# Performance work log

Measured on AMD Instinct MI355X. Metric: run time of the kernel, lower is better.

Reference implementation:

```python
import jax, jax.numpy as jnp
import numpy as np


def _gla_forward(hidden_state, Wq, bq, Wk, bk, Wv, bv, Wg, bg, Wo, bo):
    # hidden_state: (B, T, H)
    q = hidden_state @ Wq + bq                       # (B, T, K)
    k = jax.nn.sigmoid(hidden_state @ Wk + bk)       # (B, T, K)
    g = jax.nn.sigmoid(hidden_state @ Wg + bg)       # (B, T, K)
    v = hidden_state @ Wv + bv                       # (B, T, V)

    B = hidden_state.shape[0]
    K = Wq.shape[1]
    V = Wv.shape[1]
    state0 = jnp.zeros((B, K, V), dtype=hidden_state.dtype)

    def step(state, inp):
        q_t, k_t, g_t, v_t = inp                     # (B,K),(B,K),(B,K),(B,V)
        # state = state * gate[..., None] + k outer v
        state = state * g_t[:, :, None] + k_t[:, :, None] * v_t[:, None, :]
        out_t = jnp.einsum('bkv,bk->bv', state, q_t)  # (B, V)
        return state, out_t

    # scan over time: move T to leading axis
    xs = (jnp.swapaxes(q, 0, 1), jnp.swapaxes(k, 0, 1),
          jnp.swapaxes(g, 0, 1), jnp.swapaxes(v, 0, 1))
    final_state, outs = jax.lax.scan(step, state0, xs)  # outs: (T, B, V)
    out = jnp.swapaxes(outs, 0, 1)                      # (B, T, V)
    out = out @ Wo + bo                                 # (B, T, O)
    return out, final_state


def setup_inputs() -> dict:
    key = jax.random.key(0)
    ks = jax.random.split(key, 12)
    B, T, H, K, V, O = 8, 2048, 1024, 256, 256, 1024
    s = 0.02
    return {
        'hidden_state': jax.random.normal(ks[0], (B, T, H), dtype=jnp.float32),
        'Wq': jax.random.normal(ks[1], (H, K), dtype=jnp.float32) * s,
        'bq': jax.random.normal(ks[2], (K,), dtype=jnp.float32) * s,
        'Wk': jax.random.normal(ks[3], (H, K), dtype=jnp.float32) * s,
        'bk': jax.random.normal(ks[4], (K,), dtype=jnp.float32) * s,
        'Wv': jax.random.normal(ks[5], (H, V), dtype=jnp.float32) * s,
        'bv': jax.random.normal(ks[6], (V,), dtype=jnp.float32) * s,
        'Wg': jax.random.normal(ks[7], (H, K), dtype=jnp.float32) * s,
        'bg': jax.random.normal(ks[8], (K,), dtype=jnp.float32) * s,
        'Wo': jax.random.normal(ks[9], (V, O), dtype=jnp.float32) * s,
        'bo': jax.random.normal(ks[10], (O,), dtype=jnp.float32) * s,
    }


def reference(hidden_state, Wq, bq, Wk, bk, Wv, bv, Wg, bg, Wo, bo):
    return _gla_forward(hidden_state, Wq, bq, Wk, bk, Wv, bv, Wg, bg, Wo, bo)
```

## Files before the change

kernel.cpp:

```cpp
#include <hip/hip_runtime.h>

#define Bb 8
#define Tt 2048
#define Hh 1024
#define Kk 256
#define Vv 256
#define Oo 1024
#define CC 64
#define NC 32

typedef __attribute__((ext_vector_type(8))) __bf16 bf16x8;
typedef __attribute__((ext_vector_type(4))) float f32x4;

__device__ __forceinline__ unsigned short f2b(float f) {
  unsigned u = __float_as_uint(f);
  u = (u + 0x7FFFu + ((u >> 16) & 1u)) >> 16;
  return (unsigned short)u;
}
__device__ __forceinline__ float b2f(unsigned short u) {
  return __uint_as_float(((unsigned)u) << 16);
}
__device__ __forceinline__ void gload_lds16(const unsigned short* g, unsigned short* l) {
  __builtin_amdgcn_global_load_lds(
      (const __attribute__((address_space(1))) void*)g,
      (__attribute__((address_space(3))) void*)l, 16, 0, 0);
}

__global__ __launch_bounds__(256) void cast_bf16_kernel(const float* __restrict__ in,
                                                        unsigned short* __restrict__ out,
                                                        int n4) {
  int i = blockIdx.x * 256 + threadIdx.x;
  if (i >= n4) return;
  float4 v = ((const float4*)in)[i];
  ushort4 o;
  o.x = f2b(v.x); o.y = f2b(v.y); o.z = f2b(v.z); o.w = f2b(v.w);
  ((ushort4*)out)[i] = o;
}

__global__ __launch_bounds__(256) void transpose_cast_kernel(const float* __restrict__ W,
                                                             unsigned short* __restrict__ WT,
                                                             int H, int N) {
  __shared__ float tile[32][33];
  int h0 = blockIdx.x * 32, n0 = blockIdx.y * 32;
  int tx = threadIdx.x & 31, ty = threadIdx.x >> 5;
  for (int r = ty; r < 32; r += 8)
    tile[r][tx] = W[(size_t)(h0 + r) * N + n0 + tx];
  __syncthreads();
  for (int r = ty; r < 32; r += 8)
    WT[(size_t)(n0 + r) * H + h0 + tx] = f2b(tile[tx][r]);
}

#define BM 128
#define BN 128
#define BK 64

template <int MODE>
__global__ __launch_bounds__(256, 4) void gemm_mf_kernel(
    const unsigned short* __restrict__ A, const unsigned short* __restrict__ Bt,
    const float* __restrict__ b0p, const float* __restrict__ b1p,
    const float* __restrict__ b2p, const float* __restrict__ b3p,
    float* __restrict__ Cf,
    unsigned short* __restrict__ O0, unsigned short* __restrict__ O1,
    unsigned short* __restrict__ O2, unsigned short* __restrict__ O3,
    int M, int N, int K) {
  __shared__ __align__(16) unsigned short shbuf[16384];
  unsigned short* As = shbuf;
  unsigned short* Bs = shbuf + 8192;
  const int tid = threadIdx.x;
  const int lane = tid & 63, wid = tid >> 6;
  const int wm = wid >> 1, wn = wid & 1;
  const int lin = blockIdx.x + blockIdx.y * gridDim.x;
  const int xcd = lin & 7;
  const int jj = lin >> 3;
  const int mpg = gridDim.y >> 3;
  const int m0 = (xcd * mpg + jj / gridDim.x) * BM;
  const int n0 = (jj % gridDim.x) * BN;
  const int fr = lane & 15, fq = lane >> 4;
  const int srl = lane >> 3;
  const int scs = ((lane & 7) ^ srl) * 8;
  const unsigned short* gaBase = A + (size_t)(m0 + srl) * K + scs;
  const unsigned short* gbBase = Bt + (size_t)(n0 + srl) * K + scs;

  f32x4 acc[4][4] = {};
  const int nt = K / BK;
  for (int t = 0; t < nt; ++t) {
    const int k0 = t * BK;
    __syncthreads();
#pragma unroll
    for (int inst = 0; inst < 4; ++inst) {
      const int rb = wid * 32 + inst * 8;
      gload_lds16(gaBase + (size_t)rb * K + k0, &As[rb * BK]);
      gload_lds16(gbBase + (size_t)rb * K + k0, &Bs[rb * BK]);
    }
    __syncthreads();
#pragma unroll
    for (int ks = 0; ks < 2; ++ks) {
      bf16x8 af[4], bfv[4];
#pragma unroll
      for (int j = 0; j < 4; ++j) {
        const int R = wn * 64 + j * 16 + fr;
        const int ch = ((ks << 2) | fq) ^ (fr & 7);
        bfv[j] = *(const bf16x8*)&Bs[R * BK + ch * 8];
      }
#pragma unroll
      for (int i = 0; i < 4; ++i) {
        const int R = wm * 64 + i * 16 + fr;
        const int ch = ((ks << 2) | fq) ^ (fr & 7);
        af[i] = *(const bf16x8*)&As[R * BK + ch * 8];
      }
#pragma unroll
      for (int i = 0; i < 4; ++i)
#pragma unroll
        for (int j = 0; j < 4; ++j)
          acc[i][j] = __builtin_amdgcn_mfma_f32_16x16x32_bf16(af[i], bfv[j], acc[i][j], 0, 0, 0);
    }
  }
  if (MODE == 1) {
#pragma unroll
    for (int j = 0; j < 4; ++j) {
      const int n = n0 + wn * 64 + j * 16 + fr;
      const float bv = b0p[n];
#pragma unroll
      for (int i = 0; i < 4; ++i) {
        const int mb = m0 + wm * 64 + i * 16 + fq * 4;
#pragma unroll
        for (int r = 0; r < 4; ++r)
          Cf[(size_t)(mb + r) * N + n] = acc[i][j][r] + bv;
      }
    }
  } else {
    __syncthreads();
    const int sel = n0 >> 8;
    const float* bp = sel == 0 ? b0p : sel == 1 ? b1p : sel == 2 ? b2p : b3p;
#pragma unroll
    for (int j = 0; j < 4; ++j) {
      const int ncol = wn * 64 + j * 16 + fr;
      const int nloc = (n0 & 255) + ncol;
      const float bv = bp[nloc];
#pragma unroll
      for (int i = 0; i < 4; ++i) {
#pragma unroll
        for (int r = 0; r < 4; ++r) {
          const int ml = wm * 64 + i * 16 + fq * 4 + r;
          const float x = acc[i][j][r] + bv;
          unsigned short us;
          if (sel == 0) {
            us = f2b(x);
          } else if (sel == 1) {
            us = f2b(1.f / (1.f + expf(-x)));
          } else if (sel == 2) {
            float e = exp2f(-x * 1.44269504f);
            float lg = -log2f(1.f + e);
            _Float16 hv = (_Float16)lg;
            __builtin_memcpy(&us, &hv, 2);
          } else {
            us = f2b(x);
          }
          if (sel == 3) {
            const int cm = (ml >> 3) ^ (ncol & 15);
            shbuf[ncol * 128 + cm * 8 + (ml & 7)] = us;
          } else {
            const int cn = (ncol >> 3) ^ (ml & 15);
            shbuf[ml * 128 + cn * 8 + (ncol & 7)] = us;
          }
        }
      }
    }
    __syncthreads();
    const int row = tid >> 1;
    const int half = tid & 1;
    if (sel == 3) {
      unsigned short* dst = O3 + ((size_t)(m0 >> 11) * Vv + (n0 & 255) + row) * Tt +
                            (m0 & 2047) + half * 64;
#pragma unroll
      for (int ic = 0; ic < 8; ++ic) {
        const int chunk = half * 8 + ic;
        const int sc = chunk ^ (row & 15);
        *(uint4*)(dst + ic * 8) = *(const uint4*)&shbuf[row * 128 + sc * 8];
      }
    } else {
      unsigned short* Op = sel == 0 ? O0 : sel == 1 ? O1 : O2;
      unsigned short* dst = Op + (size_t)(m0 + row) * 256 + (n0 & 255) + half * 64;
#pragma unroll
      for (int ic = 0; ic < 8; ++ic) {
        const int chunk = half * 8 + ic;
        const int sc = chunk ^ (row & 15);
        *(uint4*)(dst + ic * 8) = *(const uint4*)&shbuf[row * 128 + sc * 8];
      }
    }
  }
}

__global__ __launch_bounds__(256) void prep_sgemm_kernel(
    const unsigned short* __restrict__ qb, const unsigned short* __restrict__ kb,
    const unsigned short* __restrict__ lgb, const unsigned short* __restrict__ vTb,
    unsigned short* __restrict__ q2b, unsigned short* __restrict__ qab,
    unsigned short* __restrict__ kab,
    float* __restrict__ LBb, float* __restrict__ Dendb,
    unsigned short* __restrict__ Sb) {
  __shared__ __align__(16) unsigned short khs[256][72];
  const int c = blockIdx.x, b = blockIdx.y;
  const int k = threadIdx.x;
  const int task = b * NC + c;
  const size_t rowbase = ((size_t)b * Tt + (size_t)c * CC) * Kk + k;
  float Ls = 0.f;
  float LBr[4];
#pragma unroll
  for (int gq = 0; gq < 4; ++gq) {
    LBr[gq] = Ls;
#pragma unroll
    for (int tt = 0; tt < 16; ++tt) {
      int t = gq * 16 + tt;
      _Float16 hv;
      __builtin_memcpy(&hv, &lgb[rowbase + (size_t)t * Kk], 2);
      Ls += (float)hv;
    }
  }
  const float Lend = Ls;
#pragma unroll
  for (int gq = 0; gq < 4; ++gq) LBb[(size_t)task * 1024 + gq * 256 + k] = LBr[gq];
  Dendb[task * 256 + k] = exp2f(Lend);
  float L = 0.f;
#pragma unroll
  for (int gq = 0; gq < 4; ++gq) {
    const float LBc = LBr[gq];
    unsigned kw[8];
#pragma unroll
    for (int tt = 0; tt < 16; ++tt) {
      int t = gq * 16 + tt;
      size_t off = rowbase + (size_t)t * Kk;
      _Float16 hv;
      __builtin_memcpy(&hv, &lgb[off], 2);
      L += (float)hv;
      float qv = b2f(qb[off]);
      float kv = b2f(kb[off]);
      q2b[off] = f2b(qv * exp2f(L));
      qab[off] = f2b(qv * exp2f(L - LBc));
      kab[off] = f2b(kv * exp2f(LBc - L));
      unsigned short kh = f2b(kv * exp2f(Lend - L));
      if (tt & 1) kw[tt >> 1] |= ((unsigned)kh) << 16;
      else        kw[tt >> 1] = kh;
    }
    uint4 u0; u0.x = kw[0]; u0.y = kw[1]; u0.z = kw[2]; u0.w = kw[3];
    uint4 u1; u1.x = kw[4]; u1.y = kw[5]; u1.z = kw[6]; u1.w = kw[7];
    *(uint4*)&khs[k][gq * 16] = u0;
    *(uint4*)&khs[k][gq * 16 + 8] = u1;
  }
  __syncthreads();
  const int tid = threadIdx.x, lane = tid & 63, w = tid >> 6;
  const int fr = lane & 15, fq = lane >> 4, fk = fq * 8;
  const unsigned short* vt = vTb + (size_t)b * (Vv * Tt) + (size_t)c * CC;
  for (int vb4 = 0; vb4 < 4; ++vb4) {
    f32x4 acc[4][4] = {};
#pragma unroll
    for (int ks = 0; ks < 2; ++ks) {
      bf16x8 af[4], bf[4];
#pragma unroll
      for (int i = 0; i < 4; ++i)
        af[i] = *(const bf16x8*)&khs[w * 64 + i * 16 + fr][ks * 32 + fk];
#pragma unroll
      for (int j = 0; j < 4; ++j)
        bf[j] = *(const bf16x8*)(vt + (size_t)(vb4 * 64 + j * 16 + fr) * Tt + ks * 32 + fk);
#pragma unroll
      for (int i = 0; i < 4; ++i)
#pragma unroll
        for (int j = 0; j < 4; ++j)
          acc[i][j] = __builtin_amdgcn_mfma_f32_16x16x32_bf16(af[i], bf[j], acc[i][j], 0, 0, 0);
    }
#pragma unroll
    for (int i = 0; i < 4; ++i)
#pragma unroll
      for (int j = 0; j < 4; ++j)
#pragma unroll
        for (int r = 0; r < 4; ++r)
          Sb[(size_t)task * (Kk * Vv) + (size_t)(w * 64 + i * 16 + fq * 4 + r) * Vv +
             vb4 * 64 + j * 16 + fr] = f2b(acc[i][j][r]);
  }
}

__global__ __launch_bounds__(256) void passR_kernel(
    const unsigned short* __restrict__ Sb, const float* __restrict__ Dendb,
    unsigned short* __restrict__ S0Tb, float* __restrict__ state_out) {
  const int vt = blockIdx.x, kt = blockIdx.y, b = blockIdx.z;
  const int tid = threadIdx.x;
  const int kq = tid >> 2;
  const int vq = tid & 3;
  const int vr = tid >> 3;
  const int kqq = tid & 7;
  __shared__ __align__(16) unsigned short Ts[32][72];
  float st[8];
#pragma unroll
  for (int j = 0; j < 8; ++j) st[j] = 0.f;
  for (int c = 0; c < NC; ++c) {
    const int task = b * NC + c;
#pragma unroll
    for (int j = 0; j < 8; ++j) Ts[vq * 8 + j][kq] = f2b(st[j]);
    __syncthreads();
    {
      unsigned short* dst = S0Tb + (size_t)task * (Kk * Vv) +
                            (size_t)(vt * 32 + vr) * Kk + kt * 64 + kqq * 8;
      *(uint4*)dst = *(const uint4*)&Ts[vr][kqq * 8];
    }
    __syncthreads();
    const float d = Dendb[task * 256 + kt * 64 + kq];
    const unsigned short* sp = Sb + (size_t)task * (Kk * Vv) +
                               (size_t)(kt * 64 + kq) * Vv + vt * 32 + vq * 8;
    uint4 raw = *(const uint4*)sp;
    unsigned ws_[4] = {raw.x, raw.y, raw.z, raw.w};
#pragma unroll
    for (int e = 0; e < 4; ++e) {
      float lo = __uint_as_float(ws_[e] << 16);
      float hi = __uint_as_float(ws_[e] & 0xFFFF0000u);
      st[e * 2]     = d * st[e * 2] + lo;
      st[e * 2 + 1] = d * st[e * 2 + 1] + hi;
    }
  }
  float* so = state_out + (size_t)(b * Kk + kt * 64 + kq) * Vv + vt * 32 + vq * 8;
#pragma unroll
  for (int j = 0; j < 8; ++j) so[j] = st[j];
}

__global__ __launch_bounds__(256) void passO_kernel(
    const unsigned short* __restrict__ qab, const unsigned short* __restrict__ kab,
    const unsigned short* __restrict__ q2b, const float* __restrict__ LBb,
    const unsigned short* __restrict__ S0Tb, const unsigned short* __restrict__ vTb,
    unsigned short* __restrict__ attb) {
  const int c = blockIdx.x, b = blockIdx.y;
  const int task = b * NC + c;
  const int tid = threadIdx.x, lane = tid & 63, w = tid >> 6;
  const int fr = lane & 15, fq = lane >> 4, fk = fq * 8;
  __shared__ float LB_s[4][256];
  __shared__ float D_s[6][256];
  __shared__ __align__(16) unsigned short A_s[64][72];
  const size_t tbase = (size_t)task * (CC * Kk);
  for (int idx = tid; idx < 1024; idx += 256) LB_s[idx >> 8][idx & 255] = LBb[(size_t)task * 1024 + idx];
  for (int idx = tid; idx < 64 * 72 / 2; idx += 256) ((unsigned*)A_s)[idx] = 0;
  __syncthreads();
  {
    const int kk = tid;
#pragma unroll
    for (int pi = 0; pi < 6; ++pi) {
      const int I = (pi >= 3) ? 3 : (pi >= 1) ? 2 : 1;
      const int J = pi - (I * (I - 1)) / 2;
      D_s[pi][kk] = exp2f(LB_s[I][kk] - LB_s[J][kk]);
    }
  }
  __syncthreads();
  for (int p = w; p < 10; p += 4) {
    const int I = (p >= 6) ? 3 : (p >= 3) ? 2 : (p >= 1) ? 1 : 0;
    const int J = p - (I * (I + 1)) / 2;
    const int pidx = (I * (I - 1)) / 2 + J;
    f32x4 acc = {0.f, 0.f, 0.f, 0.f};
#pragma unroll
    for (int ks = 0; ks < 8; ++ks) {
      const int k0 = ks * 32 + fk;
      bf16x8 af = *(const bf16x8*)(qab + tbase + (size_t)(I * 16 + fr) * Kk + k0);
      if (I != J) {
#pragma unroll
        for (int e = 0; e < 8; ++e)
          af[e] = (__bf16)((float)af[e] * D_s[pidx][k0 + e]);
      }
      bf16x8 bf = *(const bf16x8*)(kab + tbase + (size_t)(J * 16 + fr) * Kk + k0);
      acc = __builtin_amdgcn_mfma_f32_16x16x32_bf16(af, bf, acc, 0, 0, 0);
    }
#pragma unroll
    for (int r = 0; r < 4; ++r) {
      const int ml = fq * 4 + r, nl = fr;
      bool keep = (I != J) || (nl <= ml);
      A_s[I * 16 + ml][J * 16 + nl] = keep ? f2b(acc[r]) : (unsigned short)0;
    }
  }
  __syncthreads();
  f32x4 acc2[4][4] = {};
  const unsigned short* q2t = q2b + tbase;
  const unsigned short* s0t = S0Tb + (size_t)task * (Kk * Vv);
  const unsigned short* vtp = vTb + (size_t)b * (Vv * Tt) + (size_t)c * CC;
  const int vbase = w * 64;
#pragma unroll
  for (int ks = 0; ks < 8; ++ks) {
    const int k0 = ks * 32 + fk;
    bf16x8 af[4], bf[4];
#pragma unroll
    for (int i = 0; i < 4; ++i) af[i] = *(const bf16x8*)(q2t + (size_t)(i * 16 + fr) * Kk + k0);
#pragma unroll
    for (int j = 0; j < 4; ++j) bf[j] = *(const bf16x8*)(s0t + (size_t)(vbase + j * 16 + fr) * Kk + k0);
#pragma unroll
    for (int i = 0; i < 4; ++i)
#pragma unroll
      for (int j = 0; j < 4; ++j)
        acc2[i][j] = __builtin_amdgcn_mfma_f32_16x16x32_bf16(af[i], bf[j], acc2[i][j], 0, 0, 0);
  }
#pragma unroll
  for (int ks = 0; ks < 2; ++ks) {
    const int s0 = ks * 32 + fk;
    bf16x8 af[4], bf[4];
#pragma unroll
    for (int i = 0; i < 4; ++i) af[i] = *(const bf16x8*)&A_s[i * 16 + fr][s0];
#pragma unroll
    for (int j = 0; j < 4; ++j) bf[j] = *(const bf16x8*)(vtp + (size_t)(vbase + j * 16 + fr) * Tt + s0);
#pragma unroll
    for (int i = 0; i < 4; ++i)
#pragma unroll
      for (int j = 0; j < 4; ++j)
        acc2[i][j] = __builtin_amdgcn_mfma_f32_16x16x32_bf16(af[i], bf[j], acc2[i][j], 0, 0, 0);
  }
#pragma unroll
  for (int i = 0; i < 4; ++i)
#pragma unroll
    for (int j = 0; j < 4; ++j)
#pragma unroll
      for (int r = 0; r < 4; ++r)
        attb[((size_t)b * Tt + c * CC + i * 16 + fq * 4 + r) * Vv + vbase + j * 16 + fr]
            = f2b(acc2[i][j][r]);
}

extern "C" void kernel_launch(void* const* d_in, const int* in_sizes, int n_in,
                              void* d_out, int out_size, void* d_ws, size_t ws_size,
                              hipStream_t stream) {
  const float* hs = (const float*)d_in[0];
  const float* Wq = (const float*)d_in[1];
  const float* bq = (const float*)d_in[2];
  const float* Wk = (const float*)d_in[3];
  const float* bk = (const float*)d_in[4];
  const float* Wv = (const float*)d_in[5];
  const float* bv = (const float*)d_in[6];
  const float* Wg = (const float*)d_in[7];
  const float* bg = (const float*)d_in[8];
  const float* Wo = (const float*)d_in[9];
  const float* bo = (const float*)d_in[10];

  float* out = (float*)d_out;
  float* state_out = out + (size_t)Bb * Tt * Oo;

  char* p = (char*)d_ws;
  auto alloc = [&](size_t bytes) {
    char* r = p;
    p += (bytes + 255) & ~(size_t)255;
    return r;
  };
  unsigned short* hsb   = (unsigned short*)alloc((size_t)Bb * Tt * Hh * 2);
  unsigned short* WallT = (unsigned short*)alloc((size_t)1024 * Hh * 2);
  unsigned short* WoT   = (unsigned short*)alloc((size_t)Oo * Vv * 2);
  unsigned short* qb    = (unsigned short*)alloc((size_t)Bb * Tt * Kk * 2);
  unsigned short* kb    = (unsigned short*)alloc((size_t)Bb * Tt * Kk * 2);
  unsigned short* lgb   = (unsigned short*)alloc((size_t)Bb * Tt * Kk * 2);
  unsigned short* vTb   = (unsigned short*)alloc((size_t)Bb * Vv * Tt * 2);
  unsigned short* attb  = (unsigned short*)alloc((size_t)Bb * Tt * Vv * 2);
  unsigned short* q2b   = (unsigned short*)alloc((size_t)Bb * Tt * Kk * 2);
  unsigned short* qab   = (unsigned short*)alloc((size_t)Bb * Tt * Kk * 2);
  unsigned short* kab   = (unsigned short*)alloc((size_t)Bb * Tt * Kk * 2);
  float*          LBb   = (float*)alloc((size_t)Bb * NC * 4 * Kk * 4);
  float*          Dendb = (float*)alloc((size_t)Bb * NC * Kk * 4);
  unsigned short* Sb    = (unsigned short*)alloc((size_t)Bb * NC * Kk * Vv * 2);
  unsigned short* S0Tb  = (unsigned short*)alloc((size_t)Bb * NC * Kk * Vv * 2);

  int n4 = Bb * Tt * Hh / 4;
  cast_bf16_kernel<<<(n4 + 255) / 256, 256, 0, stream>>>(hs, hsb, n4);
  transpose_cast_kernel<<<dim3(Hh / 32, Kk / 32), 256, 0, stream>>>(Wq, WallT + 0 * Kk * Hh, Hh, Kk);
  transpose_cast_kernel<<<dim3(Hh / 32, Kk / 32), 256, 0, stream>>>(Wk, WallT + 1 * Kk * Hh, Hh, Kk);
  transpose_cast_kernel<<<dim3(Hh / 32, Kk / 32), 256, 0, stream>>>(Wg, WallT + 2 * Kk * Hh, Hh, Kk);
  transpose_cast_kernel<<<dim3(Hh / 32, Kk / 32), 256, 0, stream>>>(Wv, WallT + 3 * Kk * Hh, Hh, Kk);
  transpose_cast_kernel<<<dim3(Vv / 32, Oo / 32), 256, 0, stream>>>(Wo, WoT, Vv, Oo);

  gemm_mf_kernel<0><<<dim3(1024 / BN, (Bb * Tt) / BM), 256, 0, stream>>>(
      hsb, WallT, bq, bk, bg, bv, nullptr, qb, kb, lgb, vTb, Bb * Tt, 1024, Hh);

  prep_sgemm_kernel<<<dim3(NC, Bb), 256, 0, stream>>>(qb, kb, lgb, vTb, q2b, qab, kab,
                                                      LBb, Dendb, Sb);

  passR_kernel<<<dim3(Vv / 32, Kk / 64, Bb), 256, 0, stream>>>(Sb, Dendb, S0Tb, state_out);

  passO_kernel<<<dim3(NC, Bb), 256, 0, stream>>>(qab, kab, q2b, LBb, S0Tb, vTb, attb);

  gemm_mf_kernel<1><<<dim3(Oo / BN, (Bb * Tt) / BM), 256, 0, stream>>>(
      attb, WoT, bo, nullptr, nullptr, nullptr, out, nullptr, nullptr, nullptr, nullptr,
      Bb * Tt, Oo, Vv);
}
```

Baseline: 218.5 us.

## Rewrite projection GEMM as 8-wave 256x128 tile with triple-buffered async loads

The bf16 MFMA GEMM now uses 512-thread blocks computing 256x128 tiles. Global-to-LDS loads go into a three-slot ring buffer prefetched two K-steps ahead, split into two halves interleaved with MFMA phases. Explicit vmcnt waits, barriers and setprio raise MFMA issue priority. The aim is to hide load latency and raise data reuse per block, at the cost of 144KB LDS per block, lower occupancy, and halved grid size for these GEMMs.

Result: slower. 265.9 us (+21.7%).

```diff
diff --git a/kernel.cpp b/kernel.cpp
--- a/kernel.cpp
+++ b/kernel.cpp
@@ -50,12 +50,12 @@
     WT[(size_t)(n0 + r) * H + h0 + tx] = f2b(tile[tx][r]);
 }
 
-#define BM 128
+#define BM 256
 #define BN 128
 #define BK 64
 
 template <int MODE>
-__global__ __launch_bounds__(256, 4) void gemm_mf_kernel(
+__global__ __launch_bounds__(512, 2) void gemm8_kernel(
     const unsigned short* __restrict__ A, const unsigned short* __restrict__ Bt,
     const float* __restrict__ b0p, const float* __restrict__ b1p,
     const float* __restrict__ b2p, const float* __restrict__ b3p,
@@ -63,9 +63,9 @@
     unsigned short* __restrict__ O0, unsigned short* __restrict__ O1,
     unsigned short* __restrict__ O2, unsigned short* __restrict__ O3,
     int M, int N, int K) {
-  __shared__ __align__(16) unsigned short shbuf[16384];
-  unsigned short* As = shbuf;
-  unsigned short* Bs = shbuf + 8192;
+  __shared__ __align__(16) unsigned short shbuf[73728];
+  unsigned short* shA = shbuf;
+  unsigned short* shB = shbuf + 49152;
   const int tid = threadIdx.x;
   const int lane = tid & 63, wid = tid >> 6;
   const int wm = wid >> 1, wn = wid & 1;
@@ -80,41 +80,81 @@
   const int scs = ((lane & 7) ^ srl) * 8;
   const unsigned short* gaBase = A + (size_t)(m0 + srl) * K + scs;
   const unsigned short* gbBase = Bt + (size_t)(n0 + srl) * K + scs;
+  const int nt = K / BK;
+
+#define SA(q, tt, slot)                                                       \
+  gload_lds16(gaBase + (size_t)((q) * 64 + wid * 8) * K + (size_t)(tt) * BK,  \
+              shA + (slot) * 16384 + ((q) * 64 + wid * 8) * 64)
+#define SB(h, tt, slot)                                                       \
+  gload_lds16(gbBase + (size_t)((h) * 64 + wid * 8) * K + (size_t)(tt) * BK,  \
+              shB + (slot) * 8192 + ((h) * 64 + wid * 8) * 64)
+
+  SA(0, 0, 0); SA(1, 0, 0); SA(2, 0, 0); SA(3, 0, 0); SB(0, 0, 0); SB(1, 0, 0);
+  SA(0, 1, 1); SA(1, 1, 1); SA(2, 1, 1); SA(3, 1, 1); SB(0, 1, 1); SB(1, 1, 1);
+  asm volatile("s_waitcnt vmcnt(6)\n\ts_barrier" ::: "memory");
 
   f32x4 acc[4][4] = {};
-  const int nt = K / BK;
   for (int t = 0; t < nt; ++t) {
-    const int k0 = t * BK;
-    __syncthreads();
-#pragma unroll
-    for (int inst = 0; inst < 4; ++inst) {
-      const int rb = wid * 32 + inst * 8;
-      gload_lds16(gaBase + (size_t)rb * K + k0, &As[rb * BK]);
-      gload_lds16(gbBase + (size_t)rb * K + k0, &Bs[rb * BK]);
-    }
-    __syncthreads();
-#pragma unroll
-    for (int ks = 0; ks < 2; ++ks) {
-      bf16x8 af[4], bfv[4];
-#pragma unroll
-      for (int j = 0; j < 4; ++j) {
-        const int R = wn * 64 + j * 16 + fr;
-        const int ch = ((ks << 2) | fq) ^ (fr & 7);
-        bfv[j] = *(const bf16x8*)&Bs[R * BK + ch * 8];
-      }
-#pragma unroll
-      for (int i = 0; i < 4; ++i) {
-        const int R = wm * 64 + i * 16 + fr;
-        const int ch = ((ks << 2) | fq) ^ (fr & 7);
-        af[i] = *(const bf16x8*)&As[R * BK + ch * 8];
-      }
-#pragma unroll
-      for (int i = 0; i < 4; ++i)
-#pragma unroll
-        for (int j = 0; j < 4; ++j)
-          acc[i][j] = __builtin_amdgcn_mfma_f32_16x16x32_bf16(af[i], bfv[j], acc[i][j], 0, 0, 0);
-    }
-  }
+    const int scur = t % 3;
+    const int spre = (t + 2) % 3;
+    const bool dstage = (t + 2) < nt;
+    const unsigned short* As = shA + scur * 16384;
+    const unsigned short* Bsl = shB + scur * 8192;
+    bf16x8 af[4][2], bfv[2][2];
+    if (dstage) { SA(0, t + 2, spre); SA(1, t + 2, spre); SB(0, t + 2, spre); }
+#pragma unroll
+    for (int i = 0; i < 4; ++i) {
+      const int r = wm * 64 + i * 16 + fr;
+#pragma unroll
+      for (int ks = 0; ks < 2; ++ks)
+        af[i][ks] = *(const bf16x8*)&As[r * 64 + (((ks << 2) | fq) ^ (r & 7)) * 8];
+    }
+#pragma unroll
+    for (int jx = 0; jx < 2; ++jx) {
+      const int cc = wn * 64 + jx * 16 + fr;
+#pragma unroll
+      for (int ks = 0; ks < 2; ++ks)
+        bfv[jx][ks] = *(const bf16x8*)&Bsl[cc * 64 + (((ks << 2) | fq) ^ (cc & 7)) * 8];
+    }
+    asm volatile("s_waitcnt lgkmcnt(0)" ::: "memory");
+    __builtin_amdgcn_sched_barrier(0);
+    __builtin_amdgcn_s_setprio(1);
+#pragma unroll
+    for (int i = 0; i < 4; ++i)
+#pragma unroll
+      for (int jx = 0; jx < 2; ++jx)
+#pragma unroll
+        for (int ks = 0; ks < 2; ++ks)
+          acc[i][jx] = __builtin_amdgcn_mfma_f32_16x16x32_bf16(af[i][ks], bfv[jx][ks],
+                                                               acc[i][jx], 0, 0, 0);
+    __builtin_amdgcn_s_setprio(0);
+    asm volatile("s_barrier" ::: "memory");
+    if (dstage) { SA(2, t + 2, spre); SA(3, t + 2, spre); SB(1, t + 2, spre); }
+#pragma unroll
+    for (int jx = 0; jx < 2; ++jx) {
+      const int cc = wn * 64 + (2 + jx) * 16 + fr;
+#pragma unroll
+      for (int ks = 0; ks < 2; ++ks)
+        bfv[jx][ks] = *(const bf16x8*)&Bsl[cc * 64 + (((ks << 2) | fq) ^ (cc & 7)) * 8];
+    }
+    asm volatile("s_waitcnt lgkmcnt(0)" ::: "memory");
+    __builtin_amdgcn_sched_barrier(0);
+    __builtin_amdgcn_s_setprio(1);
+#pragma unroll
+    for (int i = 0; i < 4; ++i)
+#pragma unroll
+      for (int jx = 0; jx < 2; ++jx)
+#pragma unroll
+        for (int ks = 0; ks < 2; ++ks)
+          acc[i][2 + jx] = __builtin_amdgcn_mfma_f32_16x16x32_bf16(af[i][ks], bfv[jx][ks],
+                                                                   acc[i][2 + jx], 0, 0, 0);
+    __builtin_amdgcn_s_setprio(0);
+    if (dstage) asm volatile("s_waitcnt vmcnt(6)\n\ts_barrier" ::: "memory");
+    else        asm volatile("s_waitcnt vmcnt(0)\n\ts_barrier" ::: "memory");
+  }
+#undef SA
+#undef SB
+
   if (MODE == 1) {
 #pragma unroll
     for (int j = 0; j < 4; ++j) {
@@ -129,14 +169,12 @@
       }
     }
   } else {
-    __syncthreads();
     const int sel = n0 >> 8;
     const float* bp = sel == 0 ? b0p : sel == 1 ? b1p : sel == 2 ? b2p : b3p;
 #pragma unroll
     for (int j = 0; j < 4; ++j) {
       const int ncol = wn * 64 + j * 16 + fr;
-      const int nloc = (n0 & 255) + ncol;
-      const float bv = bp[nloc];
+      const float bv = bp[(n0 & 255) + ncol];
 #pragma unroll
       for (int i = 0; i < 4; ++i) {
 #pragma unroll
@@ -157,8 +195,8 @@
             us = f2b(x);
           }
           if (sel == 3) {
-            const int cm = (ml >> 3) ^ (ncol & 15);
-            shbuf[ncol * 128 + cm * 8 + (ml & 7)] = us;
+            const int cm = (ml >> 3) ^ (ncol & 31);
+            shbuf[ncol * 256 + cm * 8 + (ml & 7)] = us;
           } else {
             const int cn = (ncol >> 3) ^ (ml & 15);
             shbuf[ml * 128 + cn * 8 + (ncol & 7)] = us;
@@ -167,19 +205,21 @@
       }
     }
     __syncthreads();
-    const int row = tid >> 1;
-    const int half = tid & 1;
     if (sel == 3) {
+      const int row = tid >> 2;
+      const int q4 = tid & 3;
       unsigned short* dst = O3 + ((size_t)(m0 >> 11) * Vv + (n0 & 255) + row) * Tt +
-                            (m0 & 2047) + half * 64;
+                            (m0 & 2047) + q4 * 64;
 #pragma unroll
       for (int ic = 0; ic < 8; ++ic) {
-        const int chunk = half * 8 + ic;
-        const int sc = chunk ^ (row & 15);
-        *(uint4*)(dst + ic * 8) = *(const uint4*)&shbuf[row * 128 + sc * 8];
+        const int chunk = q4 * 8 + ic;
+        const int sc = chunk ^ (row & 31);
+        *(uint4*)(dst + ic * 8) = *(const uint4*)&shbuf[row * 256 + sc * 8];
       }
     } else {
       unsigned short* Op = sel == 0 ? O0 : sel == 1 ? O1 : O2;
+      const int row = tid >> 1;
+      const int half = tid & 1;
       unsigned short* dst = Op + (size_t)(m0 + row) * 256 + (n0 & 255) + half * 64;
 #pragma unroll
       for (int ic = 0; ic < 8; ++ic) {
@@ -462,7 +502,7 @@
   transpose_cast_kernel<<<dim3(Hh / 32, Kk / 32), 256, 0, stream>>>(Wv, WallT + 3 * Kk * Hh, Hh, Kk);
   transpose_cast_kernel<<<dim3(Vv / 32, Oo / 32), 256, 0, stream>>>(Wo, WoT, Vv, Oo);
 
-  gemm_mf_kernel<0><<<dim3(1024 / BN, (Bb * Tt) / BM), 256, 0, stream>>>(
+  gemm8_kernel<0><<<dim3(1024 / BN, (Bb * Tt) / BM), 512, 0, stream>>>(
       hsb, WallT, bq, bk, bg, bv, nullptr, qb, kb, lgb, vTb, Bb * Tt, 1024, Hh);
 
   prep_sgemm_kernel<<<dim3(NC, Bb), 256, 0, stream>>>(qb, kb, lgb, vTb, q2b, qab, kab,
@@ -472,7 +512,7 @@
 
   passO_kernel<<<dim3(NC, Bb), 256, 0, stream>>>(qab, kab, q2b, LBb, S0Tb, vTb, attb);
 
-  gemm_mf_kernel<1><<<dim3(Oo / BN, (Bb * Tt) / BM), 256, 0, stream>>>(
+  gemm8_kernel<1><<<dim3(Oo / BN, (Bb * Tt) / BM), 512, 0, stream>>>(
       attb, WoT, bo, nullptr, nullptr, nullptr, out, nullptr, nullptr, nullptr, nullptr,
       Bb * Tt, Oo, Vv);
 }
```

## Split GEMM into persistent two-tile projection kernel and LDS-staged output epilogue

Applied to the files above, without the earlier changes.

The projection GEMM now launches 512 blocks, each computing two M-tiles in sequence with a fixed XCD-aware mapping, instead of one tile per block over a 1024-block grid. The output GEMM gets its own kernel that stages the fp32 result through shared memory in two halves and writes rows with coalesced float4 stores, replacing scattered scalar stores. The aim is better L2 locality and less launch or tail cost for the projection, and wider store transactions for the output. The cost is more LDS use and extra barriers in the epilogue, plus less parallelism per launch for the projection.

After: 293.4 us. +34.3%, slower.

```diff
diff --git a/kernel.cpp b/kernel.cpp
--- a/kernel.cpp
+++ b/kernel.cpp
@@ -54,89 +54,73 @@
 #define BN 128
 #define BK 64
 
-template <int MODE>
-__global__ __launch_bounds__(256, 4) void gemm_mf_kernel(
+__global__ __launch_bounds__(256, 4) void gemm_proj_kernel(
     const unsigned short* __restrict__ A, const unsigned short* __restrict__ Bt,
     const float* __restrict__ b0p, const float* __restrict__ b1p,
     const float* __restrict__ b2p, const float* __restrict__ b3p,
-    float* __restrict__ Cf,
     unsigned short* __restrict__ O0, unsigned short* __restrict__ O1,
     unsigned short* __restrict__ O2, unsigned short* __restrict__ O3,
-    int M, int N, int K) {
+    int K) {
   __shared__ __align__(16) unsigned short shbuf[16384];
   unsigned short* As = shbuf;
   unsigned short* Bs = shbuf + 8192;
   const int tid = threadIdx.x;
   const int lane = tid & 63, wid = tid >> 6;
   const int wm = wid >> 1, wn = wid & 1;
-  const int lin = blockIdx.x + blockIdx.y * gridDim.x;
+  const int lin = blockIdx.x;
   const int xcd = lin & 7;
-  const int jj = lin >> 3;
-  const int mpg = gridDim.y >> 3;
-  const int m0 = (xcd * mpg + jj / gridDim.x) * BM;
-  const int n0 = (jj % gridDim.x) * BN;
+  const int rem = lin >> 3;
+  const int jm = rem & 7, jn = rem >> 3;
+  const int n0 = jn * 128;
+  const int sel = n0 >> 8;
+  const float* bp = sel == 0 ? b0p : sel == 1 ? b1p : sel == 2 ? b2p : b3p;
   const int fr = lane & 15, fq = lane >> 4;
   const int srl = lane >> 3;
   const int scs = ((lane & 7) ^ srl) * 8;
-  const unsigned short* gaBase = A + (size_t)(m0 + srl) * K + scs;
-  const unsigned short* gbBase = Bt + (size_t)(n0 + srl) * K + scs;
-
-  f32x4 acc[4][4] = {};
   const int nt = K / BK;
-  for (int t = 0; t < nt; ++t) {
-    const int k0 = t * BK;
-    __syncthreads();
-#pragma unroll
-    for (int inst = 0; inst < 4; ++inst) {
-      const int rb = wid * 32 + inst * 8;
-      gload_lds16(gaBase + (size_t)rb * K + k0, &As[rb * BK]);
-      gload_lds16(gbBase + (size_t)rb * K + k0, &Bs[rb * BK]);
-    }
-    __syncthreads();
-#pragma unroll
-    for (int ks = 0; ks < 2; ++ks) {
-      bf16x8 af[4], bfv[4];
-#pragma unroll
-      for (int j = 0; j < 4; ++j) {
-        const int R = wn * 64 + j * 16 + fr;
-        const int ch = ((ks << 2) | fq) ^ (fr & 7);
-        bfv[j] = *(const bf16x8*)&Bs[R * BK + ch * 8];
-      }
-#pragma unroll
-      for (int i = 0; i < 4; ++i) {
-        const int R = wm * 64 + i * 16 + fr;
-        const int ch = ((ks << 2) | fq) ^ (fr & 7);
-        af[i] = *(const bf16x8*)&As[R * BK + ch * 8];
-      }
-#pragma unroll
-      for (int i = 0; i < 4; ++i)
-#pragma unroll
-        for (int j = 0; j < 4; ++j)
-          acc[i][j] = __builtin_amdgcn_mfma_f32_16x16x32_bf16(af[i], bfv[j], acc[i][j], 0, 0, 0);
-    }
-  }
-  if (MODE == 1) {
-#pragma unroll
-    for (int j = 0; j < 4; ++j) {
-      const int n = n0 + wn * 64 + j * 16 + fr;
-      const float bv = b0p[n];
-#pragma unroll
-      for (int i = 0; i < 4; ++i) {
-        const int mb = m0 + wm * 64 + i * 16 + fq * 4;
-#pragma unroll
-        for (int r = 0; r < 4; ++r)
-          Cf[(size_t)(mb + r) * N + n] = acc[i][j][r] + bv;
-      }
-    }
-  } else {
-    __syncthreads();
-    const int sel = n0 >> 8;
-    const float* bp = sel == 0 ? b0p : sel == 1 ? b1p : sel == 2 ? b2p : b3p;
+
+  for (int h = 0; h < 2; ++h) {
+    const int m0 = (xcd * 16 + h * 8 + jm) * BM;
+    const unsigned short* gaBase = A + (size_t)(m0 + srl) * K + scs;
+    const unsigned short* gbBase = Bt + (size_t)(n0 + srl) * K + scs;
+    f32x4 acc[4][4] = {};
+    for (int t = 0; t < nt; ++t) {
+      const int k0 = t * BK;
+      __syncthreads();
+#pragma unroll
+      for (int inst = 0; inst < 4; ++inst) {
+        const int rb = wid * 32 + inst * 8;
+        gload_lds16(gaBase + (size_t)rb * K + k0, &As[rb * BK]);
+        gload_lds16(gbBase + (size_t)rb * K + k0, &Bs[rb * BK]);
+      }
+      __syncthreads();
+#pragma unroll
+      for (int ks = 0; ks < 2; ++ks) {
+        bf16x8 af[4], bfv[4];
+#pragma unroll
+        for (int j = 0; j < 4; ++j) {
+          const int R = wn * 64 + j * 16 + fr;
+          const int ch = ((ks << 2) | fq) ^ (fr & 7);
+          bfv[j] = *(const bf16x8*)&Bs[R * BK + ch * 8];
+        }
+#pragma unroll
+        for (int i = 0; i < 4; ++i) {
+          const int R = wm * 64 + i * 16 + fr;
+          const int ch = ((ks << 2) | fq) ^ (fr & 7);
+          af[i] = *(const bf16x8*)&As[R * BK + ch * 8];
+        }
+#pragma unroll
+        for (int i = 0; i < 4; ++i)
+#pragma unroll
+          for (int j = 0; j < 4; ++j)
+            acc[i][j] = __builtin_amdgcn_mfma_f32_16x16x32_bf16(af[i], bfv[j], acc[i][j], 0, 0, 0);
+      }
+    }
+    __syncthreads();
 #pragma unroll
     for (int j = 0; j < 4; ++j) {
       const int ncol = wn * 64 + j * 16 + fr;
-      const int nloc = (n0 & 255) + ncol;
-      const float bv = bp[nloc];
+      const float bv = bp[(n0 & 255) + ncol];
 #pragma unroll
       for (int i = 0; i < 4; ++i) {
 #pragma unroll
@@ -191,6 +175,86 @@
   }
 }
 
+__global__ __launch_bounds__(256, 4) void gemm_out_kernel(
+    const unsigned short* __restrict__ A, const unsigned short* __restrict__ Bt,
+    const float* __restrict__ bias, float* __restrict__ Cf,
+    int M, int N, int K) {
+  __shared__ __align__(16) float fstage[8448];
+  unsigned short* As = (unsigned short*)fstage;
+  unsigned short* Bs = As + 8192;
+  const int tid = threadIdx.x;
+  const int lane = tid & 63, wid = tid >> 6;
+  const int wm = wid >> 1, wn = wid & 1;
+  const int lin = blockIdx.x + blockIdx.y * gridDim.x;
+  const int xcd = lin & 7;
+  const int jj = lin >> 3;
+  const int mpg = gridDim.y >> 3;
+  const int m0 = (xcd * mpg + jj / gridDim.x) * BM;
+  const int n0 = (jj % gridDim.x) * BN;
+  const int fr = lane & 15, fq = lane >> 4;
+  const int srl = lane >> 3;
+  const int scs = ((lane & 7) ^ srl) * 8;
+  const unsigned short* gaBase = A + (size_t)(m0 + srl) * K + scs;
+  const unsigned short* gbBase = Bt + (size_t)(n0 + srl) * K + scs;
+
+  f32x4 acc[4][4] = {};
+  const int nt = K / BK;
+  for (int t = 0; t < nt; ++t) {
+    const int k0 = t * BK;
+    __syncthreads();
+#pragma unroll
+    for (int inst = 0; inst < 4; ++inst) {
+      const int rb = wid * 32 + inst * 8;
+      gload_lds16(gaBase + (size_t)rb * K + k0, &As[rb * BK]);
+      gload_lds16(gbBase + (size_t)rb * K + k0, &Bs[rb * BK]);
+    }
+    __syncthreads();
+#pragma unroll
+    for (int ks = 0; ks < 2; ++ks) {
+      bf16x8 af[4], bfv[4];
+#pragma unroll
+      for (int j = 0; j < 4; ++j) {
+        const int R = wn * 64 + j * 16 + fr;
+        const int ch = ((ks << 2) | fq) ^ (fr & 7);
+        bfv[j] = *(const bf16x8*)&Bs[R * BK + ch * 8];
+      }
+#pragma unroll
+      for (int i = 0; i < 4; ++i) {
+        const int R = wm * 64 + i * 16 + fr;
+        const int ch = ((ks << 2) | fq) ^ (fr & 7);
+        af[i] = *(const bf16x8*)&As[R * BK + ch * 8];
+      }
+#pragma unroll
+      for (int i = 0; i < 4; ++i)
+#pragma unroll
+        for (int j = 0; j < 4; ++j)
+          acc[i][j] = __builtin_amdgcn_mfma_f32_16x16x32_bf16(af[i], bfv[j], acc[i][j], 0, 0, 0);
+    }
+  }
+  for (int ch = 0; ch < 2; ++ch) {
+    __syncthreads();
+    if (wm == ch) {
+#pragma unroll
+      for (int j = 0; j < 4; ++j) {
+        const int col = wn * 64 + j * 16 + fr;
+        const float bv = bias[n0 + col];
+#pragma unroll
+        for (int i = 0; i < 4; ++i)
+#pragma unroll
+          for (int r = 0; r < 4; ++r)
+            fstage[(i * 16 + fq * 4 + r) * 132 + col] = acc[i][j][r] + bv;
+      }
+    }
+    __syncthreads();
+    const int rl = tid >> 2, qc = tid & 3;
+    float* dst = Cf + (size_t)(m0 + ch * 64 + rl) * N + n0 + qc * 32;
+    const float* src = fstage + rl * 132 + qc * 32;
+#pragma unroll
+    for (int e = 0; e < 8; ++e)
+      *(float4*)(dst + e * 4) = *(const float4*)(src + e * 4);
+  }
+}
+
 __global__ __launch_bounds__(256) void prep_sgemm_kernel(
     const unsigned short* __restrict__ qb, const unsigned short* __restrict__ kb,
     const unsigned short* __restrict__ lgb, const unsigned short* __restrict__ vTb,
@@ -462,8 +526,8 @@
   transpose_cast_kernel<<<dim3(Hh / 32, Kk / 32), 256, 0, stream>>>(Wv, WallT + 3 * Kk * Hh, Hh, Kk);
   transpose_cast_kernel<<<dim3(Vv / 32, Oo / 32), 256, 0, stream>>>(Wo, WoT, Vv, Oo);
 
-  gemm_mf_kernel<0><<<dim3(1024 / BN, (Bb * Tt) / BM), 256, 0, stream>>>(
-      hsb, WallT, bq, bk, bg, bv, nullptr, qb, kb, lgb, vTb, Bb * Tt, 1024, Hh);
+  gemm_proj_kernel<<<512, 256, 0, stream>>>(
+      hsb, WallT, bq, bk, bg, bv, qb, kb, lgb, vTb, Hh);
 
   prep_sgemm_kernel<<<dim3(NC, Bb), 256, 0, stream>>>(qb, kb, lgb, vTb, q2b, qab, kab,
                                                       LBb, Dendb, Sb);
@@ -472,7 +536,6 @@
 
   passO_kernel<<<dim3(NC, Bb), 256, 0, stream>>>(qab, kab, q2b, LBb, S0Tb, vTb, attb);
 
-  gemm_mf_kernel<1><<<dim3(Oo / BN, (Bb * Tt) / BM), 256, 0, stream>>>(
-      attb, WoT, bo, nullptr, nullptr, nullptr, out, nullptr, nullptr, nullptr, nullptr,
-      Bb * Tt, Oo, Vv);
-}
+  gemm_out_kernel<<<dim3(Oo / BN, (Bb * Tt) / BM), 256, 0, stream>>>(
+      attb, WoT, bo, out, Bb * Tt, Oo, Vv);
+}
```

## Double-buffer GEMM LDS tiles with BK=32 to overlap global loads with MFMA

Applied to the files above, without the earlier changes.

The bf16 MFMA GEMM now uses a K-tile of 32 and two LDS buffers in the same shared allocation. The next tile is prefetched with global_load_lds while the current one is consumed, using vmcnt waits and raw s_barrier instead of two __syncthreads per step. The swizzle is reworked for the narrower tile. The aim is to hide global-to-LDS latency, at the cost of twice as many loop iterations and tighter reliance on hand-written waitcnt ordering.

Result: slower. 223.5 us (+2.3%).

```diff
diff --git a/kernel.cpp b/kernel.cpp
--- a/kernel.cpp
+++ b/kernel.cpp
@@ -52,7 +52,7 @@
 
 #define BM 128
 #define BN 128
-#define BK 64
+#define BK 32
 
 template <int MODE>
 __global__ __launch_bounds__(256, 4) void gemm_mf_kernel(
@@ -76,37 +76,46 @@
   const int m0 = (xcd * mpg + jj / gridDim.x) * BM;
   const int n0 = (jj % gridDim.x) * BN;
   const int fr = lane & 15, fq = lane >> 4;
-  const int srl = lane >> 3;
-  const int scs = ((lane & 7) ^ srl) * 8;
+  const int srl = lane >> 2;
+  const int scs = ((lane & 3) ^ (srl & 3)) * 8;
   const unsigned short* gaBase = A + (size_t)(m0 + srl) * K + scs;
   const unsigned short* gbBase = Bt + (size_t)(n0 + srl) * K + scs;
+  const int nt = K / BK;
+
+#define STAGE(buf, tt)                                                         \
+  {                                                                            \
+    _Pragma("unroll") for (int inst = 0; inst < 2; ++inst) {                   \
+      const int rb = wid * 32 + inst * 16;                                     \
+      gload_lds16(gaBase + (size_t)rb * K + (size_t)(tt) * BK,                 \
+                  &As[(buf) * 4096 + rb * BK]);                                \
+      gload_lds16(gbBase + (size_t)rb * K + (size_t)(tt) * BK,                 \
+                  &Bs[(buf) * 4096 + rb * BK]);                                \
+    }                                                                          \
+  }
 
   f32x4 acc[4][4] = {};
-  const int nt = K / BK;
+  STAGE(0, 0);
+  int cur = 0;
   for (int t = 0; t < nt; ++t) {
-    const int k0 = t * BK;
-    __syncthreads();
-#pragma unroll
-    for (int inst = 0; inst < 4; ++inst) {
-      const int rb = wid * 32 + inst * 8;
-      gload_lds16(gaBase + (size_t)rb * K + k0, &As[rb * BK]);
-      gload_lds16(gbBase + (size_t)rb * K + k0, &Bs[rb * BK]);
-    }
-    __syncthreads();
-#pragma unroll
-    for (int ks = 0; ks < 2; ++ks) {
+    if (t + 1 < nt) {
+      STAGE(cur ^ 1, t + 1);
+      asm volatile("s_waitcnt vmcnt(4)\n\ts_barrier" ::: "memory");
+    } else {
+      asm volatile("s_waitcnt vmcnt(0)\n\ts_barrier" ::: "memory");
+    }
+    {
       bf16x8 af[4], bfv[4];
 #pragma unroll
       for (int j = 0; j < 4; ++j) {
         const int R = wn * 64 + j * 16 + fr;
-        const int ch = ((ks << 2) | fq) ^ (fr & 7);
-        bfv[j] = *(const bf16x8*)&Bs[R * BK + ch * 8];
+        const int ch = fq ^ (R & 3);
+        bfv[j] = *(const bf16x8*)&Bs[cur * 4096 + R * BK + ch * 8];
       }
 #pragma unroll
       for (int i = 0; i < 4; ++i) {
         const int R = wm * 64 + i * 16 + fr;
-        const int ch = ((ks << 2) | fq) ^ (fr & 7);
-        af[i] = *(const bf16x8*)&As[R * BK + ch * 8];
+        const int ch = fq ^ (R & 3);
+        af[i] = *(const bf16x8*)&As[cur * 4096 + R * BK + ch * 8];
       }
 #pragma unroll
       for (int i = 0; i < 4; ++i)
@@ -114,7 +123,11 @@
         for (int j = 0; j < 4; ++j)
           acc[i][j] = __builtin_amdgcn_mfma_f32_16x16x32_bf16(af[i], bfv[j], acc[i][j], 0, 0, 0);
     }
-  }
+    asm volatile("s_barrier" ::: "memory");
+    cur ^= 1;
+  }
+#undef STAGE
+
   if (MODE == 1) {
 #pragma unroll
     for (int j = 0; j < 4; ++j) {
@@ -129,14 +142,12 @@
       }
     }
   } else {
-    __syncthreads();
     const int sel = n0 >> 8;
     const float* bp = sel == 0 ? b0p : sel == 1 ? b1p : sel == 2 ? b2p : b3p;
 #pragma unroll
     for (int j = 0; j < 4; ++j) {
       const int ncol = wn * 64 + j * 16 + fr;
-      const int nloc = (n0 & 255) + ncol;
-      const float bv = bp[nloc];
+      const float bv = bp[(n0 & 255) + ncol];
 #pragma unroll
       for (int i = 0; i < 4; ++i) {
 #pragma unroll
```
